# Performance work log

Hardware: AMD Instinct MI355X
Metric: run time of the kernel (lower is better)

## Reference

```python
import jax, jax.numpy as jnp
import numpy as np

EMBED_DIM = 768
NUM_HEADS = 12
HEAD_DIM = EMBED_DIM // NUM_HEADS


def setup_inputs() -> dict:
    key = jax.random.key(0)
    ks = jax.random.split(key, 9)
    B, S, D = 2, 2048, EMBED_DIM
    scale = 1.0 / np.sqrt(D)
    x = jax.random.normal(ks[0], (B, S, D), dtype=jnp.float32)
    Wq = jax.random.normal(ks[1], (D, D), dtype=jnp.float32) * scale
    bq = jax.random.normal(ks[2], (D,), dtype=jnp.float32) * 0.01
    Wk = jax.random.normal(ks[3], (D, D), dtype=jnp.float32) * scale
    bk = jax.random.normal(ks[4], (D,), dtype=jnp.float32) * 0.01
    Wv = jax.random.normal(ks[5], (D, D), dtype=jnp.float32) * scale
    bv = jax.random.normal(ks[6], (D,), dtype=jnp.float32) * 0.01
    Wo = jax.random.normal(ks[7], (D, D), dtype=jnp.float32) * scale
    bo = jax.random.normal(ks[8], (D,), dtype=jnp.float32) * 0.01
    return {"x": x, "Wq": Wq, "bq": bq, "Wk": Wk, "bk": bk,
            "Wv": Wv, "bv": bv, "Wo": Wo, "bo": bo}


def reference(x, Wq, bq, Wk, bk, Wv, bv, Wo, bo):
    B, S, D = x.shape
    H, hd = NUM_HEADS, HEAD_DIM
    # projections (torch Linear: x @ W^T + b; here W stored as (D,D) used directly)
    q = (x @ Wq + bq).reshape(B, S, H, hd).transpose(0, 2, 1, 3)  # (B,H,S,hd)
    k = (x @ Wk + bk).reshape(B, S, H, hd).transpose(0, 2, 1, 3)
    v = (x @ Wv + bv).reshape(B, S, H, hd).transpose(0, 2, 1, 3)
    scores = jnp.einsum('bhqd,bhkd->bhqk', q, k) / jnp.sqrt(jnp.float32(hd))
    attn = jax.nn.softmax(scores, axis=-1)                        # (B,H,S,S)
    out = jnp.einsum('bhqk,bhkd->bhqd', attn, v)                  # (B,H,S,hd)
    out = out.transpose(0, 2, 1, 3).reshape(B, S, D)
    return out @ Wo + bo
```

## Files before the change

### kernel.cpp

```cpp
#include <hip/hip_runtime.h>
#include <hip/hip_bf16.h>

#define NHEADS 12
#define HDIM 64
#define BATCH 2
#define SEQ 2048
#define DMODEL 768
#define MROWS (BATCH * SEQ)

typedef __bf16  bf16x8 __attribute__((ext_vector_type(8)));
typedef float   f32x4  __attribute__((ext_vector_type(4)));

__device__ inline unsigned short to_bf16(float f) {
    union { float f; unsigned u; } x; x.f = f;
    const unsigned r = x.u + 0x7FFFu + ((x.u >> 16) & 1u);
    return (unsigned short)(r >> 16);
}
__device__ inline unsigned pack_bf16x2(float a, float b) {
    const __hip_bfloat162 h = __float22bfloat162_rn(float2{a, b});
    union { __hip_bfloat162 h; unsigned u; } c; c.h = h; return c.u;
}

#define GLDS16(gsrc, ldst)                                                    \
    __builtin_amdgcn_global_load_lds(                                         \
        (const __attribute__((address_space(1))) void*)(gsrc),                \
        (__attribute__((address_space(3))) void*)(ldst), 16, 0, 0)

__global__ __launch_bounds__(256) void cvt_x(const float* __restrict__ in,
                                             unsigned short* __restrict__ out,
                                             int n4) {
    const int i = blockIdx.x * 256 + threadIdx.x;
    if (i < n4) {
        const float4 v = reinterpret_cast<const float4*>(in)[i];
        ushort4 o;
        o.x = to_bf16(v.x); o.y = to_bf16(v.y);
        o.z = to_bf16(v.z); o.w = to_bf16(v.w);
        reinterpret_cast<ushort4*>(out)[i] = o;
    }
}

__global__ __launch_bounds__(256) void cvt_wT(const float* __restrict__ Wq,
                                              const float* __restrict__ Wk,
                                              const float* __restrict__ Wv,
                                              const float* __restrict__ Wo,
                                              unsigned short* __restrict__ wt_all,
                                              unsigned short* __restrict__ wot) {
    const int z = blockIdx.z;
    const float* W = (z == 0) ? Wq : (z == 1) ? Wk : (z == 2) ? Wv : Wo;
    unsigned short* out = (z < 3) ? (wt_all + (size_t)z * DMODEL * DMODEL) : wot;

    __shared__ float tile[32][33];
    const int tx = threadIdx.x & 31, ty = threadIdx.x >> 5;
    const int nbase = blockIdx.x * 32, kbase = blockIdx.y * 32;

    #pragma unroll
    for (int p = 0; p < 4; ++p) {
        const int r = ty + p * 8;
        tile[r][tx] = W[(size_t)(kbase + r) * DMODEL + nbase + tx];
    }
    __syncthreads();
    #pragma unroll
    for (int p = 0; p < 4; ++p) {
        const int r = ty + p * 8;
        out[(size_t)(nbase + r) * DMODEL + kbase + tx] = to_bf16(tile[tx][r]);
    }
}

__global__ __launch_bounds__(256) void gemm_qkv(const unsigned short* __restrict__ A,
                                                const unsigned short* __restrict__ Wt,
                                                const float* __restrict__ bq,
                                                const float* __restrict__ bk,
                                                const float* __restrict__ bv,
                                                unsigned short* __restrict__ q_bf,
                                                unsigned short* __restrict__ k_bf,
                                                unsigned short* __restrict__ vt_bf) {
    constexpr int K = DMODEL;
    __shared__ unsigned short As[128 * 32];
    __shared__ unsigned short Bs[128 * 32];

    const int t = threadIdx.x;
    const int lane = t & 63;
    const int w = t >> 6, wr = w >> 1, wc = w & 1;
    const int m0 = blockIdx.y * 128, n0 = blockIdx.x * 128;
    const int lr = lane & 15;
    const int kg = lane >> 4;

    const int row0 = t >> 2,        cp0 = t & 3;
    const int row1 = (t + 256) >> 2, cp1 = t & 3;
    const int c0 = cp0 ^ ((row0 >> 1) & 3);
    const int c1 = cp1 ^ ((row1 >> 1) & 3);
    unsigned short* asd0 = &As[(w * 64) * 8];
    unsigned short* asd1 = &As[(256 + w * 64) * 8];
    unsigned short* bsd0 = &Bs[(w * 64) * 8];
    unsigned short* bsd1 = &Bs[(256 + w * 64) * 8];

    f32x4 acc[4][4] = {};

    for (int k0 = 0; k0 < K; k0 += 32) {
        GLDS16(A  + (size_t)(m0 + row0) * K + k0 + c0 * 8, asd0);
        GLDS16(A  + (size_t)(m0 + row1) * K + k0 + c1 * 8, asd1);
        GLDS16(Wt + (size_t)(n0 + row0) * K + k0 + c0 * 8, bsd0);
        GLDS16(Wt + (size_t)(n0 + row1) * K + k0 + c1 * 8, bsd1);
        __syncthreads();

        bf16x8 af[4], bfr[4];
        #pragma unroll
        for (int i = 0; i < 4; ++i) {
            const int ar = wr * 64 + i * 16 + lr;
            af[i] = *reinterpret_cast<const bf16x8*>(
                &As[ar * 32 + ((kg ^ ((ar >> 1) & 3)) * 8)]);
            const int br = wc * 64 + i * 16 + lr;
            bfr[i] = *reinterpret_cast<const bf16x8*>(
                &Bs[br * 32 + ((kg ^ ((br >> 1) & 3)) * 8)]);
        }
        #pragma unroll
        for (int i = 0; i < 4; ++i)
            #pragma unroll
            for (int j = 0; j < 4; ++j)
                acc[i][j] = __builtin_amdgcn_mfma_f32_16x16x32_bf16(
                    af[i], bfr[j], acc[i][j], 0, 0, 0);
        __syncthreads();
    }

    const int seg = n0 / DMODEL;
    const float scale = (seg == 0) ? 0.125f : 1.0f;
    const float* bias = (seg == 0) ? bq : (seg == 1) ? bk : bv;
    const int mb = m0 + wr * 64, nb = n0 - seg * DMODEL + wc * 64;

    #pragma unroll
    for (int i = 0; i < 4; ++i) {
        #pragma unroll
        for (int j = 0; j < 4; ++j) {
            const int cl = nb + j * 16 + lr;
            const float bv_ = bias[cl];
            const int h = cl >> 6, d = cl & (HDIM - 1);
            if (seg < 2) {
                unsigned short* dst = (seg == 0) ? q_bf : k_bf;
                #pragma unroll
                for (int q = 0; q < 4; ++q) {
                    const int row = mb + i * 16 + kg * 4 + q;
                    const int b = row >> 11, s = row & (SEQ - 1);
                    dst[(((size_t)(b * NHEADS + h)) * SEQ + s) * HDIM + d] =
                        to_bf16((acc[i][j][q] + bv_) * scale);
                }
            } else {
                ushort4 pk;
                #pragma unroll
                for (int q = 0; q < 4; ++q)
                    ((unsigned short*)&pk)[q] = to_bf16(acc[i][j][q] + bv_);
                const int r0 = mb + i * 16 + kg * 4;
                const int b = r0 >> 11, s = r0 & (SEQ - 1);
                *reinterpret_cast<ushort4*>(
                    &vt_bf[(((size_t)(b * NHEADS + h)) * HDIM + d) * SEQ + s]) = pk;
            }
        }
    }
}

__global__ __launch_bounds__(256) void gemm_out(const unsigned short* __restrict__ A,
                                                const unsigned short* __restrict__ Bt,
                                                const float* __restrict__ bias,
                                                float* __restrict__ out) {
    constexpr int K = DMODEL;
    __shared__ unsigned short As[128 * 32];
    __shared__ unsigned short Bs[128 * 32];

    const int t = threadIdx.x;
    const int lane = t & 63;
    const int w = t >> 6, wr = w >> 1, wc = w & 1;
    const int m0 = blockIdx.y * 128, n0 = blockIdx.x * 128;
    const int lr = lane & 15;
    const int kg = lane >> 4;

    const int row0 = t >> 2,        cp0 = t & 3;
    const int row1 = (t + 256) >> 2, cp1 = t & 3;
    const int c0 = cp0 ^ ((row0 >> 1) & 3);
    const int c1 = cp1 ^ ((row1 >> 1) & 3);
    unsigned short* asd0 = &As[(w * 64) * 8];
    unsigned short* asd1 = &As[(256 + w * 64) * 8];
    unsigned short* bsd0 = &Bs[(w * 64) * 8];
    unsigned short* bsd1 = &Bs[(256 + w * 64) * 8];

    f32x4 acc[4][4] = {};

    for (int k0 = 0; k0 < K; k0 += 32) {
        GLDS16(A  + (size_t)(m0 + row0) * K + k0 + c0 * 8, asd0);
        GLDS16(A  + (size_t)(m0 + row1) * K + k0 + c1 * 8, asd1);
        GLDS16(Bt + (size_t)(n0 + row0) * K + k0 + c0 * 8, bsd0);
        GLDS16(Bt + (size_t)(n0 + row1) * K + k0 + c1 * 8, bsd1);
        __syncthreads();

        bf16x8 af[4], bfr[4];
        #pragma unroll
        for (int i = 0; i < 4; ++i) {
            const int ar = wr * 64 + i * 16 + lr;
            af[i] = *reinterpret_cast<const bf16x8*>(
                &As[ar * 32 + ((kg ^ ((ar >> 1) & 3)) * 8)]);
            const int br = wc * 64 + i * 16 + lr;
            bfr[i] = *reinterpret_cast<const bf16x8*>(
                &Bs[br * 32 + ((kg ^ ((br >> 1) & 3)) * 8)]);
        }
        #pragma unroll
        for (int i = 0; i < 4; ++i)
            #pragma unroll
            for (int j = 0; j < 4; ++j)
                acc[i][j] = __builtin_amdgcn_mfma_f32_16x16x32_bf16(
                    af[i], bfr[j], acc[i][j], 0, 0, 0);
        __syncthreads();
    }

    const int mb = m0 + wr * 64, nb = n0 + wc * 64;
    #pragma unroll
    for (int i = 0; i < 4; ++i) {
        #pragma unroll
        for (int j = 0; j < 4; ++j) {
            const int col = nb + j * 16 + lr;
            const float bv = bias[col];
            #pragma unroll
            for (int q = 0; q < 4; ++q) {
                const int row = mb + i * 16 + kg * 4 + q;
                out[(size_t)row * DMODEL + col] = acc[i][j][q] + bv;
            }
        }
    }
}

__global__ __launch_bounds__(256, 4) void flash_mfma(
        const unsigned short* __restrict__ Qg,
        const unsigned short* __restrict__ Kgl,
        const unsigned short* __restrict__ Vtg,
        unsigned short* __restrict__ Cctx) {
    __shared__ __align__(16) unsigned short k_s[64 * 72];
    __shared__ __align__(16) unsigned short v_s[64 * 72];
    __shared__ __align__(16) unsigned short p_s[4 * 16 * 72];

    const int t = threadIdx.x;
    const int lane = t & 63, w = t >> 6;
    const int lr = lane & 15, kg = lane >> 4;
    const int qb = blockIdx.x, bh = blockIdx.y;
    const size_t sbase = (size_t)bh * SEQ * HDIM;
    const size_t vtb   = (size_t)bh * HDIM * SEQ;

    const int q0 = qb * 64 + w * 16;
    const bf16x8 qf0 = *reinterpret_cast<const bf16x8*>(
        &Qg[sbase + (size_t)(q0 + lr) * HDIM + kg * 8]);
    const bf16x8 qf1 = *reinterpret_cast<const bf16x8*>(
        &Qg[sbase + (size_t)(q0 + lr) * HDIM + 32 + kg * 8]);

    bf16x8 ones;
    #pragma unroll
    for (int i = 0; i < 8; ++i) ones[i] = (__bf16)1.0f;

    const int sr = t >> 2, cst = t & 3;

    uint4 kr0, kr1, vr0, vr1;
    {
        const size_t ka = sbase + (size_t)sr * HDIM;
        kr0 = *reinterpret_cast<const uint4*>(&Kgl[ka + cst * 8]);
        kr1 = *reinterpret_cast<const uint4*>(&Kgl[ka + (cst + 4) * 8]);
        const size_t va = vtb + (size_t)sr * SEQ;
        vr0 = *reinterpret_cast<const uint4*>(&Vtg[va + cst * 8]);
        vr1 = *reinterpret_cast<const uint4*>(&Vtg[va + (cst + 4) * 8]);
    }

    f32x4 oa[4] = {};
    f32x4 l_acc = {};
    float m_run[4] = {-1e30f, -1e30f, -1e30f, -1e30f};

    const int NT = SEQ / 64;
    for (int kt = 0; kt < NT; ++kt) {
        __syncthreads();
        *reinterpret_cast<uint4*>(&k_s[sr * 72 + cst * 8])       = kr0;
        *reinterpret_cast<uint4*>(&k_s[sr * 72 + (cst + 4) * 8]) = kr1;
        *reinterpret_cast<uint4*>(&v_s[sr * 72 + cst * 8])       = vr0;
        *reinterpret_cast<uint4*>(&v_s[sr * 72 + (cst + 4) * 8]) = vr1;
        __syncthreads();
        if (kt + 1 < NT) {
            const size_t ka = sbase + (size_t)((kt + 1) * 64 + sr) * HDIM;
            kr0 = *reinterpret_cast<const uint4*>(&Kgl[ka + cst * 8]);
            kr1 = *reinterpret_cast<const uint4*>(&Kgl[ka + (cst + 4) * 8]);
            const size_t va = vtb + (size_t)sr * SEQ + (kt + 1) * 64;
            vr0 = *reinterpret_cast<const uint4*>(&Vtg[va + cst * 8]);
            vr1 = *reinterpret_cast<const uint4*>(&Vtg[va + (cst + 4) * 8]);
        }

        f32x4 st[4] = {};
        __builtin_amdgcn_s_setprio(1);
        #pragma unroll
        for (int jk = 0; jk < 4; ++jk) {
            const bf16x8 kf0 = *reinterpret_cast<const bf16x8*>(
                &k_s[(jk * 16 + lr) * 72 + kg * 8]);
            const bf16x8 kf1 = *reinterpret_cast<const bf16x8*>(
                &k_s[(jk * 16 + lr) * 72 + 32 + kg * 8]);
            st[jk] = __builtin_amdgcn_mfma_f32_16x16x32_bf16(qf0, kf0, st[jk], 0, 0, 0);
            st[jk] = __builtin_amdgcn_mfma_f32_16x16x32_bf16(qf1, kf1, st[jk], 0, 0, 0);
        }
        __builtin_amdgcn_s_setprio(0);

        float mx[4];
        #pragma unroll
        for (int q = 0; q < 4; ++q)
            mx[q] = fmaxf(fmaxf(st[0][q], st[1][q]), fmaxf(st[2][q], st[3][q]));
        #pragma unroll
        for (int s = 1; s < 16; s <<= 1)
            #pragma unroll
            for (int q = 0; q < 4; ++q)
                mx[q] = fmaxf(mx[q], __shfl_xor(mx[q], s));

        float f[4];
        #pragma unroll
        for (int q = 0; q < 4; ++q) {
            const float mn = fmaxf(m_run[q], mx[q]);
            f[q] = __expf(m_run[q] - mn);
            m_run[q] = mn;
        }

        unsigned pk01[4], pk23[4];
        #pragma unroll
        for (int jk = 0; jk < 4; ++jk) {
            pk01[jk] = pack_bf16x2(__expf(st[jk][0] - m_run[0]),
                                   __expf(st[jk][1] - m_run[1]));
            pk23[jk] = pack_bf16x2(__expf(st[jk][2] - m_run[2]),
                                   __expf(st[jk][3] - m_run[3]));
        }

        #pragma unroll
        for (int q = 0; q < 4; ++q) l_acc[q] *= f[q];
        #pragma unroll
        for (int jd = 0; jd < 4; ++jd)
            #pragma unroll
            for (int q = 0; q < 4; ++q)
                oa[jd][q] *= f[q];

        const int pbase = w * (16 * 72);
        #pragma unroll
        for (int jk = 0; jk < 4; ++jk) {
            p_s[pbase + (kg * 4 + 0) * 72 + jk * 16 + lr] = (unsigned short)(pk01[jk] & 0xFFFFu);
            p_s[pbase + (kg * 4 + 1) * 72 + jk * 16 + lr] = (unsigned short)(pk01[jk] >> 16);
            p_s[pbase + (kg * 4 + 2) * 72 + jk * 16 + lr] = (unsigned short)(pk23[jk] & 0xFFFFu);
            p_s[pbase + (kg * 4 + 3) * 72 + jk * 16 + lr] = (unsigned short)(pk23[jk] >> 16);
        }
        const bf16x8 pf0 = *reinterpret_cast<const bf16x8*>(
            &p_s[pbase + lr * 72 + kg * 8]);
        const bf16x8 pf1 = *reinterpret_cast<const bf16x8*>(
            &p_s[pbase + lr * 72 + 32 + kg * 8]);

        __builtin_amdgcn_s_setprio(1);
        l_acc = __builtin_amdgcn_mfma_f32_16x16x32_bf16(pf0, ones, l_acc, 0, 0, 0);
        l_acc = __builtin_amdgcn_mfma_f32_16x16x32_bf16(pf1, ones, l_acc, 0, 0, 0);
        #pragma unroll
        for (int jd = 0; jd < 4; ++jd) {
            const bf16x8 vf0 = *reinterpret_cast<const bf16x8*>(
                &v_s[(jd * 16 + lr) * 72 + kg * 8]);
            const bf16x8 vf1 = *reinterpret_cast<const bf16x8*>(
                &v_s[(jd * 16 + lr) * 72 + 32 + kg * 8]);
            oa[jd] = __builtin_amdgcn_mfma_f32_16x16x32_bf16(pf0, vf0, oa[jd], 0, 0, 0);
            oa[jd] = __builtin_amdgcn_mfma_f32_16x16x32_bf16(pf1, vf1, oa[jd], 0, 0, 0);
        }
        __builtin_amdgcn_s_setprio(0);
    }

    const int b = bh / NHEADS, h = bh % NHEADS;
    #pragma unroll
    for (int q = 0; q < 4; ++q) {
        const float inv = 1.0f / l_acc[q];
        const int s = q0 + kg * 4 + q;
        #pragma unroll
        for (int jd = 0; jd < 4; ++jd)
            Cctx[(size_t)(b * SEQ + s) * DMODEL + h * HDIM + jd * 16 + lr] =
                to_bf16(oa[jd][q] * inv);
    }
}

extern "C" void kernel_launch(void* const* d_in, const int* in_sizes, int n_in,
                              void* d_out, int out_size, void* d_ws, size_t ws_size,
                              hipStream_t stream) {
    const float* x  = (const float*)d_in[0];
    const float* Wq = (const float*)d_in[1];
    const float* bq = (const float*)d_in[2];
    const float* Wk = (const float*)d_in[3];
    const float* bk = (const float*)d_in[4];
    const float* Wv = (const float*)d_in[5];
    const float* bv = (const float*)d_in[6];
    const float* Wo = (const float*)d_in[7];
    const float* bo = (const float*)d_in[8];
    float* out = (float*)d_out;

    const size_t MD = (size_t)MROWS * DMODEL;
    const size_t W2 = (size_t)DMODEL * DMODEL;
    unsigned short* u = (unsigned short*)d_ws;
    unsigned short* x_bf   = u;
    unsigned short* q_bf   = u + MD;
    unsigned short* k_bf   = u + 2 * MD;
    unsigned short* vt_bf  = u + 3 * MD;
    unsigned short* c_bf   = u + 4 * MD;
    unsigned short* wt_all = u + 5 * MD;
    unsigned short* wot    = wt_all + 3 * W2;

    cvt_x<<<(int)(MD / 4 + 255) / 256, 256, 0, stream>>>(x, x_bf, (int)(MD / 4));
    cvt_wT<<<dim3(24, 24, 4), 256, 0, stream>>>(Wq, Wk, Wv, Wo, wt_all, wot);

    dim3 gq(3 * DMODEL / 128, MROWS / 128);
    gemm_qkv<<<gq, 256, 0, stream>>>(x_bf, wt_all, bq, bk, bv, q_bf, k_bf, vt_bf);

    dim3 ga(SEQ / 64, BATCH * NHEADS);
    flash_mfma<<<ga, 256, 0, stream>>>(q_bf, k_bf, vt_bf, c_bf);

    dim3 gg(DMODEL / 128, MROWS / 128);
    gemm_out<<<gg, 256, 0, stream>>>(c_bf, wot, bo, out);
}
```

Baseline: 214.7 us.

## Restructure flash attention to two waves with 32 query rows each, V from global

```diff
diff --git a/kernel.cpp b/kernel.cpp
--- a/kernel.cpp
+++ b/kernel.cpp
@@ -26,32 +26,33 @@
         (const __attribute__((address_space(1))) void*)(gsrc),                \
         (__attribute__((address_space(3))) void*)(ldst), 16, 0, 0)
 
-__global__ __launch_bounds__(256) void cvt_x(const float* __restrict__ in,
-                                             unsigned short* __restrict__ out,
-                                             int n4) {
-    const int i = blockIdx.x * 256 + threadIdx.x;
-    if (i < n4) {
-        const float4 v = reinterpret_cast<const float4*>(in)[i];
+__global__ __launch_bounds__(256) void cvt_all(const float* __restrict__ x,
+                                               const float* __restrict__ Wq,
+                                               const float* __restrict__ Wk,
+                                               const float* __restrict__ Wv,
+                                               const float* __restrict__ Wo,
+                                               unsigned short* __restrict__ x_bf,
+                                               unsigned short* __restrict__ wt_all,
+                                               unsigned short* __restrict__ wot) {
+    __shared__ float tile[32][33];
+    const int bid = blockIdx.x;
+    if (bid < 3072) {
+        const int i = bid * 256 + threadIdx.x;
+        const float4 v = reinterpret_cast<const float4*>(x)[i];
         ushort4 o;
         o.x = to_bf16(v.x); o.y = to_bf16(v.y);
         o.z = to_bf16(v.z); o.w = to_bf16(v.w);
-        reinterpret_cast<ushort4*>(out)[i] = o;
-    }
-}
-
-__global__ __launch_bounds__(256) void cvt_wT(const float* __restrict__ Wq,
-                                              const float* __restrict__ Wk,
-                                              const float* __restrict__ Wv,
-                                              const float* __restrict__ Wo,
-                                              unsigned short* __restrict__ wt_all,
-                                              unsigned short* __restrict__ wot) {
-    const int z = blockIdx.z;
+        reinterpret_cast<ushort4*>(x_bf)[i] = o;
+        return;
+    }
+    const int wz = bid - 3072;
+    const int z = wz / 576, r2 = wz % 576;
+    const int bx = r2 % 24, by = r2 / 24;
     const float* W = (z == 0) ? Wq : (z == 1) ? Wk : (z == 2) ? Wv : Wo;
     unsigned short* out = (z < 3) ? (wt_all + (size_t)z * DMODEL * DMODEL) : wot;
 
-    __shared__ float tile[32][33];
     const int tx = threadIdx.x & 31, ty = threadIdx.x >> 5;
-    const int nbase = blockIdx.x * 32, kbase = blockIdx.y * 32;
+    const int nbase = bx * 32, kbase = by * 32;
 
     #pragma unroll
     for (int p = 0; p < 4; ++p) {
@@ -225,14 +226,13 @@
     }
 }
 
-__global__ __launch_bounds__(256, 4) void flash_mfma(
+__global__ __launch_bounds__(128) void flash_mfma(
         const unsigned short* __restrict__ Qg,
         const unsigned short* __restrict__ Kgl,
         const unsigned short* __restrict__ Vtg,
         unsigned short* __restrict__ Cctx) {
     __shared__ __align__(16) unsigned short k_s[64 * 72];
-    __shared__ __align__(16) unsigned short v_s[64 * 72];
-    __shared__ __align__(16) unsigned short p_s[4 * 16 * 72];
+    __shared__ __align__(16) unsigned short p_s[2 * 32 * 72];
 
     const int t = threadIdx.x;
     const int lane = t & 63, w = t >> 6;
@@ -241,50 +241,56 @@
     const size_t sbase = (size_t)bh * SEQ * HDIM;
     const size_t vtb   = (size_t)bh * HDIM * SEQ;
 
-    const int q0 = qb * 64 + w * 16;
-    const bf16x8 qf0 = *reinterpret_cast<const bf16x8*>(
-        &Qg[sbase + (size_t)(q0 + lr) * HDIM + kg * 8]);
-    const bf16x8 qf1 = *reinterpret_cast<const bf16x8*>(
-        &Qg[sbase + (size_t)(q0 + lr) * HDIM + 32 + kg * 8]);
+    const int q0 = qb * 64 + w * 32;
+    bf16x8 qf[2][2];
+    #pragma unroll
+    for (int qs = 0; qs < 2; ++qs)
+        #pragma unroll
+        for (int h2 = 0; h2 < 2; ++h2)
+            qf[qs][h2] = *reinterpret_cast<const bf16x8*>(
+                &Qg[sbase + (size_t)(q0 + qs * 16 + lr) * HDIM + h2 * 32 + kg * 8]);
 
     bf16x8 ones;
     #pragma unroll
     for (int i = 0; i < 8; ++i) ones[i] = (__bf16)1.0f;
 
-    const int sr = t >> 2, cst = t & 3;
-
-    uint4 kr0, kr1, vr0, vr1;
-    {
-        const size_t ka = sbase + (size_t)sr * HDIM;
-        kr0 = *reinterpret_cast<const uint4*>(&Kgl[ka + cst * 8]);
-        kr1 = *reinterpret_cast<const uint4*>(&Kgl[ka + (cst + 4) * 8]);
-        const size_t va = vtb + (size_t)sr * SEQ;
-        vr0 = *reinterpret_cast<const uint4*>(&Vtg[va + cst * 8]);
-        vr1 = *reinterpret_cast<const uint4*>(&Vtg[va + (cst + 4) * 8]);
-    }
-
-    f32x4 oa[4] = {};
-    f32x4 l_acc = {};
-    float m_run[4] = {-1e30f, -1e30f, -1e30f, -1e30f};
+    const int sr = t & 63, h4 = t >> 6;
+
+    uint4 kr[4];
+    #pragma unroll
+    for (int c = 0; c < 4; ++c)
+        kr[c] = *reinterpret_cast<const uint4*>(
+            &Kgl[sbase + (size_t)sr * HDIM + h4 * 32 + c * 8]);
+
+    f32x4 oa[2][4] = {};
+    f32x4 l_acc[2] = {};
+    float m_run[2][4] = {{-1e30f, -1e30f, -1e30f, -1e30f},
+                         {-1e30f, -1e30f, -1e30f, -1e30f}};
 
     const int NT = SEQ / 64;
     for (int kt = 0; kt < NT; ++kt) {
         __syncthreads();
-        *reinterpret_cast<uint4*>(&k_s[sr * 72 + cst * 8])       = kr0;
-        *reinterpret_cast<uint4*>(&k_s[sr * 72 + (cst + 4) * 8]) = kr1;
-        *reinterpret_cast<uint4*>(&v_s[sr * 72 + cst * 8])       = vr0;
-        *reinterpret_cast<uint4*>(&v_s[sr * 72 + (cst + 4) * 8]) = vr1;
-        __syncthreads();
+        #pragma unroll
+        for (int c = 0; c < 4; ++c)
+            *reinterpret_cast<uint4*>(&k_s[sr * 72 + h4 * 32 + c * 8]) = kr[c];
+        __syncthreads();
+
+        bf16x8 vf[4][2];
+        #pragma unroll
+        for (int jd = 0; jd < 4; ++jd)
+            #pragma unroll
+            for (int h2 = 0; h2 < 2; ++h2)
+                vf[jd][h2] = *reinterpret_cast<const bf16x8*>(
+                    &Vtg[vtb + (size_t)(jd * 16 + lr) * SEQ + kt * 64 + h2 * 32 + kg * 8]);
+
         if (kt + 1 < NT) {
-            const size_t ka = sbase + (size_t)((kt + 1) * 64 + sr) * HDIM;
-            kr0 = *reinterpret_cast<const uint4*>(&Kgl[ka + cst * 8]);
-            kr1 = *reinterpret_cast<const uint4*>(&Kgl[ka + (cst + 4) * 8]);
-            const size_t va = vtb + (size_t)sr * SEQ + (kt + 1) * 64;
-            vr0 = *reinterpret_cast<const uint4*>(&Vtg[va + cst * 8]);
-            vr1 = *reinterpret_cast<const uint4*>(&Vtg[va + (cst + 4) * 8]);
-        }
-
-        f32x4 st[4] = {};
+            #pragma unroll
+            for (int c = 0; c < 4; ++c)
+                kr[c] = *reinterpret_cast<const uint4*>(
+                    &Kgl[sbase + (size_t)((kt + 1) * 64 + sr) * HDIM + h4 * 32 + c * 8]);
+        }
+
+        f32x4 st[2][4] = {};
         __builtin_amdgcn_s_setprio(1);
         #pragma unroll
         for (int jk = 0; jk < 4; ++jk) {
@@ -292,84 +298,104 @@
                 &k_s[(jk * 16 + lr) * 72 + kg * 8]);
             const bf16x8 kf1 = *reinterpret_cast<const bf16x8*>(
                 &k_s[(jk * 16 + lr) * 72 + 32 + kg * 8]);
-            st[jk] = __builtin_amdgcn_mfma_f32_16x16x32_bf16(qf0, kf0, st[jk], 0, 0, 0);
-            st[jk] = __builtin_amdgcn_mfma_f32_16x16x32_bf16(qf1, kf1, st[jk], 0, 0, 0);
+            #pragma unroll
+            for (int qs = 0; qs < 2; ++qs) {
+                st[qs][jk] = __builtin_amdgcn_mfma_f32_16x16x32_bf16(
+                    qf[qs][0], kf0, st[qs][jk], 0, 0, 0);
+                st[qs][jk] = __builtin_amdgcn_mfma_f32_16x16x32_bf16(
+                    qf[qs][1], kf1, st[qs][jk], 0, 0, 0);
+            }
         }
         __builtin_amdgcn_s_setprio(0);
 
-        float mx[4];
-        #pragma unroll
-        for (int q = 0; q < 4; ++q)
-            mx[q] = fmaxf(fmaxf(st[0][q], st[1][q]), fmaxf(st[2][q], st[3][q]));
-        #pragma unroll
-        for (int s = 1; s < 16; s <<= 1)
+        unsigned pk01[2][4], pk23[2][4];
+        float f[2][4];
+        #pragma unroll
+        for (int qs = 0; qs < 2; ++qs) {
+            float mx[4];
             #pragma unroll
             for (int q = 0; q < 4; ++q)
-                mx[q] = fmaxf(mx[q], __shfl_xor(mx[q], s));
-
-        float f[4];
+                mx[q] = fmaxf(fmaxf(st[qs][0][q], st[qs][1][q]),
+                              fmaxf(st[qs][2][q], st[qs][3][q]));
+            #pragma unroll
+            for (int s = 1; s < 16; s <<= 1)
+                #pragma unroll
+                for (int q = 0; q < 4; ++q)
+                    mx[q] = fmaxf(mx[q], __shfl_xor(mx[q], s));
+            #pragma unroll
+            for (int q = 0; q < 4; ++q) {
+                const float mn = fmaxf(m_run[qs][q], mx[q]);
+                f[qs][q] = __expf(m_run[qs][q] - mn);
+                m_run[qs][q] = mn;
+            }
+            #pragma unroll
+            for (int jk = 0; jk < 4; ++jk) {
+                pk01[qs][jk] = pack_bf16x2(__expf(st[qs][jk][0] - m_run[qs][0]),
+                                           __expf(st[qs][jk][1] - m_run[qs][1]));
+                pk23[qs][jk] = pack_bf16x2(__expf(st[qs][jk][2] - m_run[qs][2]),
+                                           __expf(st[qs][jk][3] - m_run[qs][3]));
+            }
+            #pragma unroll
+            for (int q = 0; q < 4; ++q) l_acc[qs][q] *= f[qs][q];
+            #pragma unroll
+            for (int jd = 0; jd < 4; ++jd)
+                #pragma unroll
+                for (int q = 0; q < 4; ++q)
+                    oa[qs][jd][q] *= f[qs][q];
+        }
+
+        const int pbase = w * (32 * 72);
+        #pragma unroll
+        for (int qs = 0; qs < 2; ++qs)
+            #pragma unroll
+            for (int jk = 0; jk < 4; ++jk) {
+                const int rb = pbase + (qs * 16 + kg * 4) * 72 + jk * 16 + lr;
+                p_s[rb]           = (unsigned short)(pk01[qs][jk] & 0xFFFFu);
+                p_s[rb + 72]      = (unsigned short)(pk01[qs][jk] >> 16);
+                p_s[rb + 144]     = (unsigned short)(pk23[qs][jk] & 0xFFFFu);
+                p_s[rb + 216]     = (unsigned short)(pk23[qs][jk] >> 16);
+            }
+        bf16x8 pf[2][2];
+        #pragma unroll
+        for (int qs = 0; qs < 2; ++qs) {
+            pf[qs][0] = *reinterpret_cast<const bf16x8*>(
+                &p_s[pbase + (qs * 16 + lr) * 72 + kg * 8]);
+            pf[qs][1] = *reinterpret_cast<const bf16x8*>(
+                &p_s[pbase + (qs * 16 + lr) * 72 + 32 + kg * 8]);
+        }
+
+        __builtin_amdgcn_s_setprio(1);
+        #pragma unroll
+        for (int qs = 0; qs < 2; ++qs) {
+            l_acc[qs] = __builtin_amdgcn_mfma_f32_16x16x32_bf16(
+                pf[qs][0], ones, l_acc[qs], 0, 0, 0);
+            l_acc[qs] = __builtin_amdgcn_mfma_f32_16x16x32_bf16(
+                pf[qs][1], ones, l_acc[qs], 0, 0, 0);
+        }
+        #pragma unroll
+        for (int jd = 0; jd < 4; ++jd)
+            #pragma unroll
+            for (int qs = 0; qs < 2; ++qs) {
+                oa[qs][jd] = __builtin_amdgcn_mfma_f32_16x16x32_bf16(
+                    pf[qs][0], vf[jd][0], oa[qs][jd], 0, 0, 0);
+                oa[qs][jd] = __builtin_amdgcn_mfma_f32_16x16x32_bf16(
+                    pf[qs][1], vf[jd][1], oa[qs][jd], 0, 0, 0);
+            }
+        __builtin_amdgcn_s_setprio(0);
+    }
+
+    const int b = bh / NHEADS, h = bh % NHEADS;
+    #pragma unroll
+    for (int qs = 0; qs < 2; ++qs)
         #pragma unroll
         for (int q = 0; q < 4; ++q) {
-            const float mn = fmaxf(m_run[q], mx[q]);
-            f[q] = __expf(m_run[q] - mn);
-            m_run[q] = mn;
-        }
-
-        unsigned pk01[4], pk23[4];
-        #pragma unroll
-        for (int jk = 0; jk < 4; ++jk) {
-            pk01[jk] = pack_bf16x2(__expf(st[jk][0] - m_run[0]),
-                                   __expf(st[jk][1] - m_run[1]));
-            pk23[jk] = pack_bf16x2(__expf(st[jk][2] - m_run[2]),
-                                   __expf(st[jk][3] - m_run[3]));
-        }
-
-        #pragma unroll
-        for (int q = 0; q < 4; ++q) l_acc[q] *= f[q];
-        #pragma unroll
-        for (int jd = 0; jd < 4; ++jd)
-            #pragma unroll
-            for (int q = 0; q < 4; ++q)
-                oa[jd][q] *= f[q];
-
-        const int pbase = w * (16 * 72);
-        #pragma unroll
-        for (int jk = 0; jk < 4; ++jk) {
-            p_s[pbase + (kg * 4 + 0) * 72 + jk * 16 + lr] = (unsigned short)(pk01[jk] & 0xFFFFu);
-            p_s[pbase + (kg * 4 + 1) * 72 + jk * 16 + lr] = (unsigned short)(pk01[jk] >> 16);
-            p_s[pbase + (kg * 4 + 2) * 72 + jk * 16 + lr] = (unsigned short)(pk23[jk] & 0xFFFFu);
-            p_s[pbase + (kg * 4 + 3) * 72 + jk * 16 + lr] = (unsigned short)(pk23[jk] >> 16);
-        }
-        const bf16x8 pf0 = *reinterpret_cast<const bf16x8*>(
-            &p_s[pbase + lr * 72 + kg * 8]);
-        const bf16x8 pf1 = *reinterpret_cast<const bf16x8*>(
-            &p_s[pbase + lr * 72 + 32 + kg * 8]);
-
-        __builtin_amdgcn_s_setprio(1);
-        l_acc = __builtin_amdgcn_mfma_f32_16x16x32_bf16(pf0, ones, l_acc, 0, 0, 0);
-        l_acc = __builtin_amdgcn_mfma_f32_16x16x32_bf16(pf1, ones, l_acc, 0, 0, 0);
-        #pragma unroll
-        for (int jd = 0; jd < 4; ++jd) {
-            const bf16x8 vf0 = *reinterpret_cast<const bf16x8*>(
-                &v_s[(jd * 16 + lr) * 72 + kg * 8]);
-            const bf16x8 vf1 = *reinterpret_cast<const bf16x8*>(
-                &v_s[(jd * 16 + lr) * 72 + 32 + kg * 8]);
-            oa[jd] = __builtin_amdgcn_mfma_f32_16x16x32_bf16(pf0, vf0, oa[jd], 0, 0, 0);
-            oa[jd] = __builtin_amdgcn_mfma_f32_16x16x32_bf16(pf1, vf1, oa[jd], 0, 0, 0);
-        }
-        __builtin_amdgcn_s_setprio(0);
-    }
-
-    const int b = bh / NHEADS, h = bh % NHEADS;
-    #pragma unroll
-    for (int q = 0; q < 4; ++q) {
-        const float inv = 1.0f / l_acc[q];
-        const int s = q0 + kg * 4 + q;
-        #pragma unroll
-        for (int jd = 0; jd < 4; ++jd)
-            Cctx[(size_t)(b * SEQ + s) * DMODEL + h * HDIM + jd * 16 + lr] =
-                to_bf16(oa[jd][q] * inv);
-    }
+            const float inv = 1.0f / l_acc[qs][q];
+            const int s = q0 + qs * 16 + kg * 4 + q;
+            #pragma unroll
+            for (int jd = 0; jd < 4; ++jd)
+                Cctx[(size_t)(b * SEQ + s) * DMODEL + h * HDIM + jd * 16 + lr] =
+                    to_bf16(oa[qs][jd][q] * inv);
+        }
 }
 
 extern "C" void kernel_launch(void* const* d_in, const int* in_sizes, int n_in,
@@ -397,14 +423,14 @@
     unsigned short* wt_all = u + 5 * MD;
     unsigned short* wot    = wt_all + 3 * W2;
 
-    cvt_x<<<(int)(MD / 4 + 255) / 256, 256, 0, stream>>>(x, x_bf, (int)(MD / 4));
-    cvt_wT<<<dim3(24, 24, 4), 256, 0, stream>>>(Wq, Wk, Wv, Wo, wt_all, wot);
+    cvt_all<<<3072 + 4 * 576, 256, 0, stream>>>(x, Wq, Wk, Wv, Wo,
+                                                x_bf, wt_all, wot);
 
     dim3 gq(3 * DMODEL / 128, MROWS / 128);
     gemm_qkv<<<gq, 256, 0, stream>>>(x_bf, wt_all, bq, bk, bv, q_bf, k_bf, vt_bf);
 
     dim3 ga(SEQ / 64, BATCH * NHEADS);
-    flash_mfma<<<ga, 256, 0, stream>>>(q_bf, k_bf, vt_bf, c_bf);
+    flash_mfma<<<ga, 128, 0, stream>>>(q_bf, k_bf, vt_bf, c_bf);
 
     dim3 gg(DMODEL / 128, MROWS / 128);
     gemm_out<<<gg, 256, 0, stream>>>(c_bf, wot, bo, out);
```

After: 252.8 us. 1.18x slower.
